# Kernel optimization log

Measured on AMD Instinct MI355X. Metric: run time of the kernel, lower is better.

The kernel has to match this reference:

```python
import jax, jax.numpy as jnp
import numpy as np

N_NODES = 100000
N_EDGES = 600000
EMB = 128
L = 5
NUM_ATOM = 119
NUM_CHIR = 3
NUM_BTYPE = 5
NUM_BDIR = 3
BN_EPS = 1e-5


def setup_inputs() -> dict:
    key = jax.random.key(0)
    ks = jax.random.split(key, 16)
    inp = {}
    inp['x'] = jax.random.randint(ks[0], (N_NODES, 2), 0, NUM_ATOM, dtype=jnp.int64 if jax.config.jax_enable_x64 else jnp.int32)
    inp['edge_index'] = jax.random.randint(ks[1], (2, N_EDGES), 0, N_NODES)
    inp['edge_attr'] = jax.random.randint(ks[2], (N_EDGES, 2), 0, NUM_BDIR)
    s = 0.05
    inp['x_emb1'] = jax.random.normal(ks[3], (NUM_ATOM, EMB), jnp.float32) * s
    inp['x_emb2'] = jax.random.normal(ks[4], (NUM_CHIR, EMB), jnp.float32) * s
    inp['edge_emb1'] = jax.random.normal(ks[5], (L, NUM_BTYPE, EMB), jnp.float32) * s
    inp['edge_emb2'] = jax.random.normal(ks[6], (L, NUM_BDIR, EMB), jnp.float32) * s
    inp['W1'] = jax.random.normal(ks[7], (L, EMB, 2 * EMB), jnp.float32) * (1.0 / np.sqrt(EMB))
    inp['b1'] = jnp.zeros((L, 2 * EMB), jnp.float32)
    inp['W2'] = jax.random.normal(ks[8], (L, 2 * EMB, EMB), jnp.float32) * (1.0 / np.sqrt(2 * EMB))
    inp['b2'] = jnp.zeros((L, EMB), jnp.float32)
    inp['eps'] = jnp.zeros((L,), jnp.float32)
    inp['gamma'] = jnp.ones((L, EMB), jnp.float32)
    inp['beta'] = jnp.zeros((L, EMB), jnp.float32)
    return inp


def reference(x, edge_index, edge_attr, x_emb1, x_emb2, edge_emb1, edge_emb2,
              W1, b1, W2, b2, eps, gamma, beta):
    N = x.shape[0]
    # node embedding: sum of two table lookups
    x0 = jnp.clip(x[:, 0], 0, x_emb1.shape[0] - 1)
    x1 = jnp.clip(x[:, 1], 0, x_emb2.shape[0] - 1)
    h = x_emb1[x0] + x_emb2[x1]  # [N, EMB]
    # add self loops (loop edge_attr = zeros -> bond type 0 / dir 0)
    loop = jnp.arange(N, dtype=edge_index.dtype)
    src = jnp.concatenate([edge_index[0], loop])  # [E+N]
    dst = jnp.concatenate([edge_index[1], loop])
    ea = jnp.concatenate([edge_attr, jnp.zeros((N, 2), dtype=edge_attr.dtype)], axis=0)
    e0 = jnp.clip(ea[:, 0], 0, edge_emb1.shape[1] - 1)
    e1 = jnp.clip(ea[:, 1], 0, edge_emb2.shape[1] - 1)
    n_layers = eps.shape[0]
    for i in range(n_layers):
        e = edge_emb1[i][e0] + edge_emb2[i][e1]              # [E+N, EMB]
        m = jax.nn.relu(h[src] + e)                           # gather + elementwise
        agg = jax.ops.segment_sum(m, dst, num_segments=N)     # scatter-add
        out = (1.0 + eps[i]) * h + agg
        # MLP: Linear -> ReLU -> Linear
        hmid = jax.nn.relu(out @ W1[i] + b1[i])
        h = hmid @ W2[i] + b2[i]
        # BatchNorm1d over nodes (batch statistics, biased variance)
        mean = jnp.mean(h, axis=0)
        var = jnp.mean((h - mean) ** 2, axis=0)
        h = (h - mean) * jax.lax.rsqrt(var + BN_EPS) * gamma[i] + beta[i]
        if i < n_layers - 1:
            h = jax.nn.relu(h)
    return h
```

## Files before the change

### kernel.cpp

```cpp
#include <hip/hip_runtime.h>

#define NN 100000
#define NPAD 100096
#define NE 600000
#define EMB 128

typedef unsigned short u16;
typedef unsigned int u32;
typedef unsigned long long u64;
typedef _Float16 half8 __attribute__((ext_vector_type(8)));
typedef float f32x4 __attribute__((ext_vector_type(4)));

__device__ __forceinline__ float4 ld4(const float* p) { return *(const float4*)p; }
__device__ __forceinline__ u32 packh2(float a, float b) {
  union { _Float16 h[2]; u32 d; } u;
  u.h[0] = (_Float16)a;
  u.h[1] = (_Float16)b;
  return u.d;
}

__global__ __launch_bounds__(256) void node_init_kernel(
    const int* __restrict__ x, const float* __restrict__ emb1,
    const float* __restrict__ emb2, _Float16* __restrict__ hb) {
  int tid = blockIdx.x * blockDim.x + threadIdx.x;
  int n = tid >> 4;
  if (n >= NN) return;
  int kc = tid & 15;
  int x0 = min(max(x[2 * n], 0), 118);
  int x1 = min(max(x[2 * n + 1], 0), 2);
  const float* p1 = emb1 + (size_t)x0 * EMB + kc * 8;
  const float* p2 = emb2 + (size_t)x1 * EMB + kc * 8;
  _Float16 o[8];
#pragma unroll
  for (int j = 0; j < 8; ++j) o[j] = (_Float16)(p1[j] + p2[j]);
  *(ulonglong2*)(hb + (size_t)n * EMB + kc * 8) = *(ulonglong2*)o;
}

__global__ __launch_bounds__(256) void hist_kernel(const int* __restrict__ ei,
                                                   int* __restrict__ deg) {
  int e = blockIdx.x * blockDim.x + threadIdx.x;
  if (e >= NE) return;
  atomicAdd(&deg[ei[NE + e]], 1);
}

__global__ __launch_bounds__(256) void scan1_kernel(const int* __restrict__ deg,
                                                    int* __restrict__ off,
                                                    int* __restrict__ bsum) {
  __shared__ int s[256];
  int t = threadIdx.x;
  int base = blockIdx.x * 1024 + t * 4;
  int v[4];
#pragma unroll
  for (int j = 0; j < 4; ++j) {
    int idx = base + j;
    v[j] = (idx < NN) ? deg[idx] : 0;
  }
  int tsum = v[0] + v[1] + v[2] + v[3];
  s[t] = tsum;
  __syncthreads();
  for (int d = 1; d < 256; d <<= 1) {
    int add = (t >= d) ? s[t - d] : 0;
    __syncthreads();
    s[t] += add;
    __syncthreads();
  }
  int run = s[t] - tsum;
#pragma unroll
  for (int j = 0; j < 4; ++j) {
    int idx = base + j;
    if (idx < NN) off[idx] = run;
    run += v[j];
  }
  if (t == 255) bsum[blockIdx.x] = s[255];
}

__global__ void scan2_kernel(int* __restrict__ bsum, int* __restrict__ off, int nb) {
  int lane = threadIdx.x;
  int v0 = (lane < nb) ? bsum[lane] : 0;
  int v1 = (lane + 64 < nb) ? bsum[lane + 64] : 0;
  int s0 = v0, s1 = v1;
  for (int d = 1; d < 64; d <<= 1) {
    int t0 = __shfl_up(s0, d);
    int t1 = __shfl_up(s1, d);
    if (lane >= d) { s0 += t0; s1 += t1; }
  }
  int tot0 = __shfl(s0, 63);
  int tot1 = __shfl(s1, 63);
  if (lane < nb) bsum[lane] = s0 - v0;
  if (lane + 64 < nb) bsum[lane + 64] = tot0 + s1 - v1;
  if (lane == 0) off[NN] = tot0 + tot1;
}

__global__ __launch_bounds__(256) void scan3_kernel(int* __restrict__ off,
                                                    const int* __restrict__ bsum) {
  int idx = blockIdx.x * blockDim.x + threadIdx.x;
  if (idx < NN) off[idx] += bsum[idx >> 10];
}

__global__ __launch_bounds__(256) void scatter_kernel(
    const int* __restrict__ ei, const int* __restrict__ ea,
    const int* __restrict__ off, int* __restrict__ cnt, int* __restrict__ csr) {
  int e = blockIdx.x * blockDim.x + threadIdx.x;
  if (e >= NE) return;
  int d = ei[NE + e];
  int s = ei[e];
  int a0 = min(max(ea[2 * e], 0), 4);
  int a1 = min(max(ea[2 * e + 1], 0), 2);
  int code = a0 * 3 + a1;
  int r = atomicAdd(&cnt[d], 1);
  csr[off[d] + r] = s | (code << 20);
}

__global__ __launch_bounds__(256) void dhist_kernel(const int* __restrict__ deg,
                                                    int* __restrict__ gbins) {
  __shared__ int l[33];
  int t = threadIdx.x;
  if (t < 33) l[t] = 0;
  __syncthreads();
  int n = blockIdx.x * 256 + t;
  if (n < NN) atomicAdd(&l[32 - min(deg[n], 32)], 1);
  __syncthreads();
  if (t < 33 && l[t]) atomicAdd(&gbins[t], l[t]);
}

__global__ void dscan_kernel(int* __restrict__ gbins) {
  int lane = threadIdx.x;
  int v = (lane < 33) ? gbins[lane] : 0;
  int s = v;
  for (int d = 1; d < 64; d <<= 1) {
    int t = __shfl_up(s, d);
    if (lane >= d) s += t;
  }
  if (lane < 33) gbins[lane] = s - v;
}

__global__ __launch_bounds__(256) void dscatter_kernel(const int* __restrict__ deg,
                                                       int* __restrict__ gbins,
                                                       int* __restrict__ perm) {
  __shared__ int lcnt[33], lbase[33];
  int t = threadIdx.x;
  if (t < 33) lcnt[t] = 0;
  __syncthreads();
  int n = blockIdx.x * 256 + t;
  int b = 0, r = 0;
  if (n < NN) {
    b = 32 - min(deg[n], 32);
    r = atomicAdd(&lcnt[b], 1);
  }
  __syncthreads();
  if (t < 33) lbase[t] = lcnt[t] ? atomicAdd(&gbins[t], lcnt[t]) : 0;
  __syncthreads();
  if (n < NN) perm[lbase[b] + r] = n;
}

__global__ __launch_bounds__(256) void combo_kernel(const float* __restrict__ ee1,
                                                    const float* __restrict__ ee2,
                                                    _Float16* __restrict__ cbh) {
  int idx = blockIdx.x * blockDim.x + threadIdx.x;
  if (idx >= 5 * 15 * 128) return;
  int l = idx / (15 * 128);
  int rem = idx % (15 * 128);
  int code = rem / 128;
  int f = rem % 128;
  cbh[idx] = (_Float16)(ee1[(l * 5 + code / 3) * 128 + f] + ee2[(l * 3 + code % 3) * 128 + f]);
}

__global__ __launch_bounds__(256) void prep_w_kernel(
    const float* __restrict__ W1g, const float* __restrict__ W2g,
    _Float16* __restrict__ W1f, _Float16* __restrict__ W2f) {
  int idx = blockIdx.x * blockDim.x + threadIdx.x;
  if (idx >= 40960) return;
  _Float16 o[8];
  if (idx < 20480) {
    int lane = idx & 63;
    int r = idx >> 6;
    int nt = r & 3, kt = (r >> 2) & 3, c = (r >> 4) & 3, l = r >> 6;
    int n = c * 64 + nt * 16 + (lane & 15);
    int kb = kt * 32 + (lane >> 4) * 8;
#pragma unroll
    for (int j = 0; j < 8; ++j) o[j] = (_Float16)W1g[((size_t)l * 128 + kb + j) * 256 + n];
    *(ulonglong2*)(W1f + (size_t)idx * 8) = *(ulonglong2*)o;
  } else {
    int i2 = idx - 20480;
    int lane = i2 & 63;
    int r = i2 >> 6;
    int nt = r & 7, ktl = (r >> 3) & 1, c = (r >> 4) & 3, l = r >> 6;
    int n = nt * 16 + (lane & 15);
    int kb = c * 64 + ktl * 32 + (lane >> 4) * 8;
#pragma unroll
    for (int j = 0; j < 8; ++j) o[j] = (_Float16)W2g[((size_t)l * 256 + kb + j) * 128 + n];
    *(ulonglong2*)(W2f + (size_t)i2 * 8) = *(ulonglong2*)o;
  }
}

template <bool NORM>
__global__ __launch_bounds__(256) void agg_kernel(
    const _Float16* __restrict__ hsrc, const float* __restrict__ scsh,
    const int* __restrict__ off, const int* __restrict__ csr,
    const _Float16* __restrict__ cbh, const float* __restrict__ epsp,
    const int* __restrict__ perm, _Float16* __restrict__ Af) {
  int tid = blockIdx.x * blockDim.x + threadIdx.x;
  int g = tid >> 4;
  int kc = tid & 15;
  float av[8] = {0.f, 0.f, 0.f, 0.f, 0.f, 0.f, 0.f, 0.f};
  float scv[8], shv[8];
  if (NORM) {
    float4 sa = ld4(scsh + kc * 8), sb = ld4(scsh + kc * 8 + 4);
    float4 ha = ld4(scsh + 128 + kc * 8), hbv = ld4(scsh + 128 + kc * 8 + 4);
    scv[0] = sa.x; scv[1] = sa.y; scv[2] = sa.z; scv[3] = sa.w;
    scv[4] = sb.x; scv[5] = sb.y; scv[6] = sb.z; scv[7] = sb.w;
    shv[0] = ha.x; shv[1] = ha.y; shv[2] = ha.z; shv[3] = ha.w;
    shv[4] = hbv.x; shv[5] = hbv.y; shv[6] = hbv.z; shv[7] = hbv.w;
  }
  int node = g;
  if (g < NN) {
    node = perm[g];
    const float eps1 = 1.0f + *epsp;
    ulonglong2 hraw = *(const ulonglong2*)(hsrc + (size_t)node * EMB + kc * 8);
    _Float16* hr = (_Float16*)&hraw;
    half8 c0 = *(const half8*)(cbh + kc * 8);
#pragma unroll
    for (int j = 0; j < 8; ++j) {
      float hv = (float)hr[j];
      if (NORM) hv = fmaxf(hv * scv[j] + shv[j], 0.f);
      av[j] = eps1 * hv + fmaxf(hv + (float)c0[j], 0.f);
    }
    int s0 = off[node], s1 = off[node + 1];
    int e = s0;
    for (; e + 3 < s1; e += 4) {
      int p0 = csr[e], p1 = csr[e + 1], p2 = csr[e + 2], p3 = csr[e + 3];
      ulonglong2 r0 = *(const ulonglong2*)(hsrc + (size_t)(p0 & 0xFFFFF) * EMB + kc * 8);
      ulonglong2 r1 = *(const ulonglong2*)(hsrc + (size_t)(p1 & 0xFFFFF) * EMB + kc * 8);
      ulonglong2 r2 = *(const ulonglong2*)(hsrc + (size_t)(p2 & 0xFFFFF) * EMB + kc * 8);
      ulonglong2 r3 = *(const ulonglong2*)(hsrc + (size_t)(p3 & 0xFFFFF) * EMB + kc * 8);
      ulonglong2 rr[4] = {r0, r1, r2, r3};
      int pp[4] = {p0, p1, p2, p3};
#pragma unroll
      for (int u = 0; u < 4; ++u) {
        half8 cc = *(const half8*)(cbh + (size_t)(pp[u] >> 20) * EMB + kc * 8);
        _Float16* sp = (_Float16*)&rr[u];
#pragma unroll
        for (int j = 0; j < 8; ++j) {
          float v = (float)sp[j];
          if (NORM) v = fmaxf(v * scv[j] + shv[j], 0.f);
          av[j] += fmaxf(v + (float)cc[j], 0.f);
        }
      }
    }
    for (; e < s1; ++e) {
      int p0 = csr[e];
      ulonglong2 r0 = *(const ulonglong2*)(hsrc + (size_t)(p0 & 0xFFFFF) * EMB + kc * 8);
      half8 cc = *(const half8*)(cbh + (size_t)(p0 >> 20) * EMB + kc * 8);
      _Float16* sp = (_Float16*)&r0;
#pragma unroll
      for (int j = 0; j < 8; ++j) {
        float v = (float)sp[j];
        if (NORM) v = fmaxf(v * scv[j] + shv[j], 0.f);
        av[j] += fmaxf(v + (float)cc[j], 0.f);
      }
    }
  }
  _Float16 o[8];
#pragma unroll
  for (int j = 0; j < 8; ++j) o[j] = (_Float16)av[j];
  *(ulonglong2*)(Af + (size_t)node * EMB + kc * 8) = *(ulonglong2*)o;
}

__global__ __launch_bounds__(256, 4) void mlp_kernel(
    const _Float16* __restrict__ Af, const _Float16* __restrict__ W1f,
    const _Float16* __restrict__ W2f,
    const float* __restrict__ b1g, const float* __restrict__ b2g,
    _Float16* __restrict__ hpre, float* __restrict__ slots) {
  __shared__ __align__(16) _Float16 Ws[16 * 64 * 8];

  const int t = threadIdx.x;
  const int w = t >> 6;
  const int lane = t & 63;
  const int q = lane >> 4, l15 = lane & 15;
  const int gw = blockIdx.x * 4 + w;
  const int n0 = gw * 16;
  float* sums = slots + (size_t)(gw & 31) * 256;

  half8 nh[4];
#pragma unroll
  for (int kt = 0; kt < 4; ++kt)
    nh[kt] = *(const half8*)(Af + (size_t)(n0 + l15) * EMB + kt * 32 + q * 8);

  f32x4 oacc[8];
#pragma unroll
  for (int a = 0; a < 8; ++a) oacc[a] = (f32x4){0.f, 0.f, 0.f, 0.f};

  const int srcA = ((q & 1) * 2) * 16 + l15;
  const int srcB = srcA + 16;
  const bool sel = (q >> 1) != 0;

  for (int c = 0; c < 4; ++c) {
    __syncthreads();
    {
      const _Float16* gb = W1f + ((size_t)(c * 16 + w * 4) * 64 + lane) * 8;
#pragma unroll
      for (int j = 0; j < 4; ++j)
        *(ulonglong2*)&Ws[(w * 4 + j) * 512 + lane * 8] =
            *(const ulonglong2*)(gb + (size_t)j * 512);
    }
    __syncthreads();

    f32x4 hacc[4];
#pragma unroll
    for (int a = 0; a < 4; ++a) hacc[a] = (f32x4){0.f, 0.f, 0.f, 0.f};
#pragma unroll
    for (int kt = 0; kt < 4; ++kt) {
#pragma unroll
      for (int colt = 0; colt < 4; ++colt) {
        half8 wh = *(const half8*)&Ws[(kt * 4 + colt) * 512 + lane * 8];
        hacc[colt] = __builtin_amdgcn_mfma_f32_16x16x32_f16(wh, nh[kt], hacc[colt], 0, 0, 0);
      }
    }
    __syncthreads();

    {
      const _Float16* gb = W2f + ((size_t)(c * 16 + w * 4) * 64 + lane) * 8;
#pragma unroll
      for (int j = 0; j < 4; ++j)
        *(ulonglong2*)&Ws[(w * 4 + j) * 512 + lane * 8] =
            *(const ulonglong2*)(gb + (size_t)j * 512);
    }

    u32 P01[4], P23[4];
#pragma unroll
    for (int colt = 0; colt < 4; ++colt) {
      float4 b1v = ld4(b1g + c * 64 + colt * 16 + q * 4);
      float v0 = fmaxf(hacc[colt][0] + b1v.x, 0.f);
      float v1 = fmaxf(hacc[colt][1] + b1v.y, 0.f);
      float v2 = fmaxf(hacc[colt][2] + b1v.z, 0.f);
      float v3 = fmaxf(hacc[colt][3] + b1v.w, 0.f);
      P01[colt] = packh2(v0, v1);
      P23[colt] = packh2(v2, v3);
    }
    __syncthreads();

#pragma unroll
    for (int ktl = 0; ktl < 2; ++ktl) {
      half8 bh;
      {
        union { u32 d[4]; half8 s; } uh;
        int c0 = 2 * ktl, c1 = 2 * ktl + 1;
        u32 a0, a1;
        a0 = (u32)__shfl((int)P01[c0], srcA); a1 = (u32)__shfl((int)P01[c1], srcA);
        uh.d[0] = sel ? a1 : a0;
        a0 = (u32)__shfl((int)P23[c0], srcA); a1 = (u32)__shfl((int)P23[c1], srcA);
        uh.d[1] = sel ? a1 : a0;
        a0 = (u32)__shfl((int)P01[c0], srcB); a1 = (u32)__shfl((int)P01[c1], srcB);
        uh.d[2] = sel ? a1 : a0;
        a0 = (u32)__shfl((int)P23[c0], srcB); a1 = (u32)__shfl((int)P23[c1], srcB);
        uh.d[3] = sel ? a1 : a0;
        bh = uh.s;
      }
#pragma unroll
      for (int nt = 0; nt < 8; ++nt) {
        half8 wh = *(const half8*)&Ws[(ktl * 8 + nt) * 512 + lane * 8];
        oacc[nt] = __builtin_amdgcn_mfma_f32_16x16x32_f16(wh, bh, oacc[nt], 0, 0, 0);
      }
    }
  }

  const int node = n0 + l15;
#pragma unroll
  for (int nt = 0; nt < 8; ++nt) {
    int ocb = nt * 16 + q * 4;
    float4 b2v = ld4(b2g + ocb);
    f32x4 s = (f32x4){0.f, 0.f, 0.f, 0.f};
    f32x4 s2 = (f32x4){0.f, 0.f, 0.f, 0.f};
    if (node < NN) {
      float v0 = oacc[nt][0] + b2v.x;
      float v1 = oacc[nt][1] + b2v.y;
      float v2 = oacc[nt][2] + b2v.z;
      float v3 = oacc[nt][3] + b2v.w;
      u64 pk = (u64)packh2(v0, v1) | ((u64)packh2(v2, v3) << 32);
      *(u64*)(hpre + (size_t)node * EMB + ocb) = pk;
      s[0] = v0; s[1] = v1; s[2] = v2; s[3] = v3;
      s2[0] = v0 * v0; s2[1] = v1 * v1; s2[2] = v2 * v2; s2[3] = v3 * v3;
    }
#pragma unroll
    for (int d = 1; d < 16; d <<= 1) {
#pragma unroll
      for (int r = 0; r < 4; ++r) {
        s[r] += __shfl_xor(s[r], d);
        s2[r] += __shfl_xor(s2[r], d);
      }
    }
    if (l15 == 0) {
#pragma unroll
      for (int r = 0; r < 4; ++r) {
        atomicAdd(&sums[ocb + r], s[r]);
        atomicAdd(&sums[128 + ocb + r], s2[r]);
      }
    }
  }
}

__global__ void stats_kernel(const float* __restrict__ slots,
                             const float* __restrict__ gamma,
                             const float* __restrict__ beta,
                             float* __restrict__ scsh) {
  int f = threadIdx.x;
  float s = 0.f, s2 = 0.f;
#pragma unroll 8
  for (int k = 0; k < 32; ++k) {
    s += slots[k * 256 + f];
    s2 += slots[k * 256 + 128 + f];
  }
  float mean = s * (1.0f / NN);
  float var = s2 * (1.0f / NN) - mean * mean;
  float sc = gamma[f] * rsqrtf(var + 1e-5f);
  scsh[f] = sc;
  scsh[128 + f] = beta[f] - mean * sc;
}

__global__ __launch_bounds__(256) void out_kernel(
    const _Float16* __restrict__ hpre, const float* __restrict__ scsh,
    float* __restrict__ out) {
  int tid = blockIdx.x * blockDim.x + threadIdx.x;
  int n = tid >> 4;
  if (n >= NN) return;
  int kc = tid & 15;
  ulonglong2 raw = *(const ulonglong2*)(hpre + (size_t)n * EMB + kc * 8);
  _Float16* hr = (_Float16*)&raw;
  float4 sa = ld4(scsh + kc * 8), sb = ld4(scsh + kc * 8 + 4);
  float4 ha = ld4(scsh + 128 + kc * 8), hbv = ld4(scsh + 128 + kc * 8 + 4);
  float scv[8] = {sa.x, sa.y, sa.z, sa.w, sb.x, sb.y, sb.z, sb.w};
  float shv[8] = {ha.x, ha.y, ha.z, ha.w, hbv.x, hbv.y, hbv.z, hbv.w};
  float v[8];
#pragma unroll
  for (int j = 0; j < 8; ++j) v[j] = (float)hr[j] * scv[j] + shv[j];
  float* d = out + (size_t)n * EMB + kc * 8;
  *(float4*)d = make_float4(v[0], v[1], v[2], v[3]);
  *(float4*)(d + 4) = make_float4(v[4], v[5], v[6], v[7]);
}

extern "C" void kernel_launch(void* const* d_in, const int* in_sizes, int n_in,
                              void* d_out, int out_size, void* d_ws, size_t ws_size,
                              hipStream_t stream) {
  const int* x = (const int*)d_in[0];
  const int* ei = (const int*)d_in[1];
  const int* ea = (const int*)d_in[2];
  const float* x_emb1 = (const float*)d_in[3];
  const float* x_emb2 = (const float*)d_in[4];
  const float* ee1 = (const float*)d_in[5];
  const float* ee2 = (const float*)d_in[6];
  const float* W1 = (const float*)d_in[7];
  const float* b1 = (const float*)d_in[8];
  const float* W2 = (const float*)d_in[9];
  const float* b2 = (const float*)d_in[10];
  const float* eps = (const float*)d_in[11];
  const float* gamma = (const float*)d_in[12];
  const float* beta = (const float*)d_in[13];
  float* out = (float*)d_out;

  float* slots = (float*)d_ws;
  float* scsh = slots + 5 * 32 * 256;
  _Float16* hpre = (_Float16*)(scsh + 5 * 256);
  _Float16* Af = hpre + (size_t)NN * EMB;
  _Float16* hb = Af + (size_t)NPAD * EMB;
  _Float16* W1f = hb + (size_t)NN * EMB;
  _Float16* W2f = W1f + 5 * 32768;
  _Float16* cbh = W2f + 5 * 32768;
  int* deg = (int*)(cbh + 5 * 15 * 128 + 64);
  int* off = deg + NN;
  int* csr = off + NN + 1;
  int* bsum = csr + NE;
  int* gbins = bsum + 128;
  int* perm = gbins + 64;

  const int NB_SCAN = (NN + 1023) / 1024;

  hipMemsetAsync(deg, 0, NN * sizeof(int), stream);
  hipMemsetAsync(gbins, 0, 64 * sizeof(int), stream);
  hipMemsetAsync(slots, 0, 5 * 32 * 256 * sizeof(float), stream);
  hist_kernel<<<(NE + 255) / 256, 256, 0, stream>>>(ei, deg);
  dhist_kernel<<<(NN + 255) / 256, 256, 0, stream>>>(deg, gbins);
  dscan_kernel<<<1, 64, 0, stream>>>(gbins);
  dscatter_kernel<<<(NN + 255) / 256, 256, 0, stream>>>(deg, gbins, perm);
  scan1_kernel<<<NB_SCAN, 256, 0, stream>>>(deg, off, bsum);
  scan2_kernel<<<1, 64, 0, stream>>>(bsum, off, NB_SCAN);
  scan3_kernel<<<(NN + 255) / 256, 256, 0, stream>>>(off, bsum);
  hipMemsetAsync(deg, 0, NN * sizeof(int), stream);
  scatter_kernel<<<(NE + 255) / 256, 256, 0, stream>>>(ei, ea, off, deg, csr);
  combo_kernel<<<(5 * 15 * 128 + 255) / 256, 256, 0, stream>>>(ee1, ee2, cbh);
  prep_w_kernel<<<160, 256, 0, stream>>>(W1, W2, W1f, W2f);
  node_init_kernel<<<NN * 16 / 256 + 1, 256, 0, stream>>>(x, x_emb1, x_emb2, hb);

  const int NBLK = NPAD / 64;
  for (int i = 0; i < 5; ++i) {
    if (i == 0)
      agg_kernel<false><<<NPAD * 16 / 256, 256, 0, stream>>>(
          hb, nullptr, off, csr, cbh + (size_t)i * 15 * EMB, eps + i, perm, Af);
    else
      agg_kernel<true><<<NPAD * 16 / 256, 256, 0, stream>>>(
          hpre, scsh + (size_t)(i - 1) * 256, off, csr,
          cbh + (size_t)i * 15 * EMB, eps + i, perm, Af);
    mlp_kernel<<<NBLK, 256, 0, stream>>>(
        Af, W1f + (size_t)i * 32768, W2f + (size_t)i * 32768,
        b1 + (size_t)i * 256, b2 + (size_t)i * 128, hpre,
        slots + (size_t)i * 32 * 256);
    stats_kernel<<<1, 128, 0, stream>>>(slots + (size_t)i * 32 * 256,
                                        gamma + (size_t)i * EMB,
                                        beta + (size_t)i * EMB,
                                        scsh + (size_t)i * 256);
  }
  out_kernel<<<NN * 16 / 256 + 1, 256, 0, stream>>>(hpre, scsh + 4 * 256, out);
}
```

Before: 644.1 us.

## Fuse preprocessing kernels, fold BN stats into consumers, drop MLP LDS weight staging

The degree-histogram, scan and permutation kernels are merged into the existing scan1/scan2/scan3 kernels, and the combo and weight prep kernels become one prep kernel. The per-layer stats kernel is removed: every block of agg_kernel and out_kernel now recomputes the BatchNorm scale and shift from the slot partial sums into shared memory. The MLP kernel no longer stages weights through LDS with barriers and reads fragments straight from global memory or L2. The aim is fewer launches and no barriers, at the cost of redundant per-block stats reduction and more global weight traffic in the MLP.

```diff
diff --git a/kernel.cpp b/kernel.cpp
--- a/kernel.cpp
+++ b/kernel.cpp
@@ -45,9 +45,12 @@
 
 __global__ __launch_bounds__(256) void scan1_kernel(const int* __restrict__ deg,
                                                     int* __restrict__ off,
-                                                    int* __restrict__ bsum) {
+                                                    int* __restrict__ bsum,
+                                                    int* __restrict__ gbins) {
   __shared__ int s[256];
+  __shared__ int l[33];
   int t = threadIdx.x;
+  if (t < 33) l[t] = 0;
   int base = blockIdx.x * 1024 + t * 4;
   int v[4];
 #pragma unroll
@@ -68,33 +71,67 @@
 #pragma unroll
   for (int j = 0; j < 4; ++j) {
     int idx = base + j;
-    if (idx < NN) off[idx] = run;
+    if (idx < NN) {
+      off[idx] = run;
+      atomicAdd(&l[32 - min(v[j], 32)], 1);
+    }
     run += v[j];
   }
   if (t == 255) bsum[blockIdx.x] = s[255];
-}
-
-__global__ void scan2_kernel(int* __restrict__ bsum, int* __restrict__ off, int nb) {
-  int lane = threadIdx.x;
-  int v0 = (lane < nb) ? bsum[lane] : 0;
-  int v1 = (lane + 64 < nb) ? bsum[lane + 64] : 0;
-  int s0 = v0, s1 = v1;
-  for (int d = 1; d < 64; d <<= 1) {
-    int t0 = __shfl_up(s0, d);
-    int t1 = __shfl_up(s1, d);
-    if (lane >= d) { s0 += t0; s1 += t1; }
-  }
-  int tot0 = __shfl(s0, 63);
-  int tot1 = __shfl(s1, 63);
-  if (lane < nb) bsum[lane] = s0 - v0;
-  if (lane + 64 < nb) bsum[lane + 64] = tot0 + s1 - v1;
-  if (lane == 0) off[NN] = tot0 + tot1;
+  __syncthreads();
+  if (t < 33 && l[t]) atomicAdd(&gbins[t], l[t]);
+}
+
+__global__ void scan2_kernel(int* __restrict__ bsum, int* __restrict__ off, int nb,
+                             int* __restrict__ gbins) {
+  int t = threadIdx.x;
+  if (t < 64) {
+    int lane = t;
+    int v0 = (lane < nb) ? bsum[lane] : 0;
+    int v1 = (lane + 64 < nb) ? bsum[lane + 64] : 0;
+    int s0 = v0, s1 = v1;
+    for (int d = 1; d < 64; d <<= 1) {
+      int t0 = __shfl_up(s0, d);
+      int t1 = __shfl_up(s1, d);
+      if (lane >= d) { s0 += t0; s1 += t1; }
+    }
+    int tot0 = __shfl(s0, 63);
+    int tot1 = __shfl(s1, 63);
+    if (lane < nb) bsum[lane] = s0 - v0;
+    if (lane + 64 < nb) bsum[lane + 64] = tot0 + s1 - v1;
+    if (lane == 0) off[NN] = tot0 + tot1;
+  } else {
+    int lane = t - 64;
+    int v = (lane < 33) ? gbins[lane] : 0;
+    int s = v;
+    for (int d = 1; d < 64; d <<= 1) {
+      int tt = __shfl_up(s, d);
+      if (lane >= d) s += tt;
+    }
+    if (lane < 33) gbins[lane] = s - v;
+  }
 }
 
 __global__ __launch_bounds__(256) void scan3_kernel(int* __restrict__ off,
-                                                    const int* __restrict__ bsum) {
-  int idx = blockIdx.x * blockDim.x + threadIdx.x;
-  if (idx < NN) off[idx] += bsum[idx >> 10];
+                                                    const int* __restrict__ bsum,
+                                                    const int* __restrict__ deg,
+                                                    int* __restrict__ gbins,
+                                                    int* __restrict__ perm) {
+  __shared__ int lcnt[33], lbase[33];
+  int t = threadIdx.x;
+  if (t < 33) lcnt[t] = 0;
+  __syncthreads();
+  int idx = blockIdx.x * 256 + t;
+  int b = 0, r = 0;
+  if (idx < NN) {
+    off[idx] += bsum[idx >> 10];
+    b = 32 - min(deg[idx], 32);
+    r = atomicAdd(&lcnt[b], 1);
+  }
+  __syncthreads();
+  if (t < 33) lbase[t] = lcnt[t] ? atomicAdd(&gbins[t], lcnt[t]) : 0;
+  __syncthreads();
+  if (idx < NN) perm[lbase[b] + r] = idx;
 }
 
 __global__ __launch_bounds__(256) void scatter_kernel(
@@ -111,65 +148,12 @@
   csr[off[d] + r] = s | (code << 20);
 }
 
-__global__ __launch_bounds__(256) void dhist_kernel(const int* __restrict__ deg,
-                                                    int* __restrict__ gbins) {
-  __shared__ int l[33];
-  int t = threadIdx.x;
-  if (t < 33) l[t] = 0;
-  __syncthreads();
-  int n = blockIdx.x * 256 + t;
-  if (n < NN) atomicAdd(&l[32 - min(deg[n], 32)], 1);
-  __syncthreads();
-  if (t < 33 && l[t]) atomicAdd(&gbins[t], l[t]);
-}
-
-__global__ void dscan_kernel(int* __restrict__ gbins) {
-  int lane = threadIdx.x;
-  int v = (lane < 33) ? gbins[lane] : 0;
-  int s = v;
-  for (int d = 1; d < 64; d <<= 1) {
-    int t = __shfl_up(s, d);
-    if (lane >= d) s += t;
-  }
-  if (lane < 33) gbins[lane] = s - v;
-}
-
-__global__ __launch_bounds__(256) void dscatter_kernel(const int* __restrict__ deg,
-                                                       int* __restrict__ gbins,
-                                                       int* __restrict__ perm) {
-  __shared__ int lcnt[33], lbase[33];
-  int t = threadIdx.x;
-  if (t < 33) lcnt[t] = 0;
-  __syncthreads();
-  int n = blockIdx.x * 256 + t;
-  int b = 0, r = 0;
-  if (n < NN) {
-    b = 32 - min(deg[n], 32);
-    r = atomicAdd(&lcnt[b], 1);
-  }
-  __syncthreads();
-  if (t < 33) lbase[t] = lcnt[t] ? atomicAdd(&gbins[t], lcnt[t]) : 0;
-  __syncthreads();
-  if (n < NN) perm[lbase[b] + r] = n;
-}
-
-__global__ __launch_bounds__(256) void combo_kernel(const float* __restrict__ ee1,
-                                                    const float* __restrict__ ee2,
-                                                    _Float16* __restrict__ cbh) {
+__global__ __launch_bounds__(256) void prep_kernel(
+    const float* __restrict__ W1g, const float* __restrict__ W2g,
+    const float* __restrict__ ee1, const float* __restrict__ ee2,
+    _Float16* __restrict__ W1f, _Float16* __restrict__ W2f,
+    _Float16* __restrict__ cbh) {
   int idx = blockIdx.x * blockDim.x + threadIdx.x;
-  if (idx >= 5 * 15 * 128) return;
-  int l = idx / (15 * 128);
-  int rem = idx % (15 * 128);
-  int code = rem / 128;
-  int f = rem % 128;
-  cbh[idx] = (_Float16)(ee1[(l * 5 + code / 3) * 128 + f] + ee2[(l * 3 + code % 3) * 128 + f]);
-}
-
-__global__ __launch_bounds__(256) void prep_w_kernel(
-    const float* __restrict__ W1g, const float* __restrict__ W2g,
-    _Float16* __restrict__ W1f, _Float16* __restrict__ W2f) {
-  int idx = blockIdx.x * blockDim.x + threadIdx.x;
-  if (idx >= 40960) return;
   _Float16 o[8];
   if (idx < 20480) {
     int lane = idx & 63;
@@ -180,7 +164,7 @@
 #pragma unroll
     for (int j = 0; j < 8; ++j) o[j] = (_Float16)W1g[((size_t)l * 128 + kb + j) * 256 + n];
     *(ulonglong2*)(W1f + (size_t)idx * 8) = *(ulonglong2*)o;
-  } else {
+  } else if (idx < 40960) {
     int i2 = idx - 20480;
     int lane = i2 & 63;
     int r = i2 >> 6;
@@ -190,27 +174,52 @@
 #pragma unroll
     for (int j = 0; j < 8; ++j) o[j] = (_Float16)W2g[((size_t)l * 256 + kb + j) * 128 + n];
     *(ulonglong2*)(W2f + (size_t)i2 * 8) = *(ulonglong2*)o;
+  } else if (idx < 40960 + 9600) {
+    int i3 = idx - 40960;
+    int l = i3 / (15 * 128);
+    int rem = i3 % (15 * 128);
+    int code = rem / 128;
+    int f = rem % 128;
+    cbh[i3] = (_Float16)(ee1[(l * 5 + code / 3) * 128 + f] + ee2[(l * 3 + code % 3) * 128 + f]);
   }
 }
 
 template <bool NORM>
 __global__ __launch_bounds__(256) void agg_kernel(
-    const _Float16* __restrict__ hsrc, const float* __restrict__ scsh,
+    const _Float16* __restrict__ hsrc, const float* __restrict__ slots,
+    const float* __restrict__ gamma, const float* __restrict__ beta,
     const int* __restrict__ off, const int* __restrict__ csr,
     const _Float16* __restrict__ cbh, const float* __restrict__ epsp,
     const int* __restrict__ perm, _Float16* __restrict__ Af) {
-  int tid = blockIdx.x * blockDim.x + threadIdx.x;
+  __shared__ float s_sc[128], s_sh[128];
+  int t = threadIdx.x;
+  if (NORM) {
+    if (t < 128) {
+      float s = 0.f, s2 = 0.f;
+#pragma unroll 8
+      for (int k = 0; k < 32; ++k) {
+        s += slots[k * 256 + t];
+        s2 += slots[k * 256 + 128 + t];
+      }
+      float mean = s * (1.0f / NN);
+      float var = s2 * (1.0f / NN) - mean * mean;
+      float sc = gamma[t] * rsqrtf(var + 1e-5f);
+      s_sc[t] = sc;
+      s_sh[t] = beta[t] - mean * sc;
+    }
+    __syncthreads();
+  }
+  int tid = blockIdx.x * blockDim.x + t;
   int g = tid >> 4;
   int kc = tid & 15;
   float av[8] = {0.f, 0.f, 0.f, 0.f, 0.f, 0.f, 0.f, 0.f};
   float scv[8], shv[8];
   if (NORM) {
-    float4 sa = ld4(scsh + kc * 8), sb = ld4(scsh + kc * 8 + 4);
-    float4 ha = ld4(scsh + 128 + kc * 8), hbv = ld4(scsh + 128 + kc * 8 + 4);
-    scv[0] = sa.x; scv[1] = sa.y; scv[2] = sa.z; scv[3] = sa.w;
-    scv[4] = sb.x; scv[5] = sb.y; scv[6] = sb.z; scv[7] = sb.w;
-    shv[0] = ha.x; shv[1] = ha.y; shv[2] = ha.z; shv[3] = ha.w;
-    shv[4] = hbv.x; shv[5] = hbv.y; shv[6] = hbv.z; shv[7] = hbv.w;
+#pragma unroll
+    for (int j = 0; j < 8; ++j) {
+      scv[j] = s_sc[kc * 8 + j];
+      shv[j] = s_sh[kc * 8 + j];
+    }
   }
   int node = g;
   if (g < NN) {
@@ -271,8 +280,6 @@
     const _Float16* __restrict__ W2f,
     const float* __restrict__ b1g, const float* __restrict__ b2g,
     _Float16* __restrict__ hpre, float* __restrict__ slots) {
-  __shared__ __align__(16) _Float16 Ws[16 * 64 * 8];
-
   const int t = threadIdx.x;
   const int w = t >> 6;
   const int lane = t & 63;
@@ -281,6 +288,9 @@
   const int n0 = gw * 16;
   float* sums = slots + (size_t)(gw & 31) * 256;
 
+  const half8* W1v = (const half8*)W1f;
+  const half8* W2v = (const half8*)W2f;
+
   half8 nh[4];
 #pragma unroll
   for (int kt = 0; kt < 4; ++kt)
@@ -294,17 +304,8 @@
   const int srcB = srcA + 16;
   const bool sel = (q >> 1) != 0;
 
+#pragma unroll
   for (int c = 0; c < 4; ++c) {
-    __syncthreads();
-    {
-      const _Float16* gb = W1f + ((size_t)(c * 16 + w * 4) * 64 + lane) * 8;
-#pragma unroll
-      for (int j = 0; j < 4; ++j)
-        *(ulonglong2*)&Ws[(w * 4 + j) * 512 + lane * 8] =
-            *(const ulonglong2*)(gb + (size_t)j * 512);
-    }
-    __syncthreads();
-
     f32x4 hacc[4];
 #pragma unroll
     for (int a = 0; a < 4; ++a) hacc[a] = (f32x4){0.f, 0.f, 0.f, 0.f};
@@ -312,18 +313,9 @@
     for (int kt = 0; kt < 4; ++kt) {
 #pragma unroll
       for (int colt = 0; colt < 4; ++colt) {
-        half8 wh = *(const half8*)&Ws[(kt * 4 + colt) * 512 + lane * 8];
+        half8 wh = W1v[(size_t)(c * 16 + kt * 4 + colt) * 64 + lane];
         hacc[colt] = __builtin_amdgcn_mfma_f32_16x16x32_f16(wh, nh[kt], hacc[colt], 0, 0, 0);
       }
-    }
-    __syncthreads();
-
-    {
-      const _Float16* gb = W2f + ((size_t)(c * 16 + w * 4) * 64 + lane) * 8;
-#pragma unroll
-      for (int j = 0; j < 4; ++j)
-        *(ulonglong2*)&Ws[(w * 4 + j) * 512 + lane * 8] =
-            *(const ulonglong2*)(gb + (size_t)j * 512);
     }
 
     u32 P01[4], P23[4];
@@ -337,7 +329,6 @@
       P01[colt] = packh2(v0, v1);
       P23[colt] = packh2(v2, v3);
     }
-    __syncthreads();
 
 #pragma unroll
     for (int ktl = 0; ktl < 2; ++ktl) {
@@ -358,7 +349,7 @@
       }
 #pragma unroll
       for (int nt = 0; nt < 8; ++nt) {
-        half8 wh = *(const half8*)&Ws[(ktl * 8 + nt) * 512 + lane * 8];
+        half8 wh = W2v[(size_t)(c * 16 + ktl * 8 + nt) * 64 + lane];
         oacc[nt] = __builtin_amdgcn_mfma_f32_16x16x32_f16(wh, bh, oacc[nt], 0, 0, 0);
       }
     }
@@ -399,40 +390,35 @@
   }
 }
 
-__global__ void stats_kernel(const float* __restrict__ slots,
-                             const float* __restrict__ gamma,
-                             const float* __restrict__ beta,
-                             float* __restrict__ scsh) {
-  int f = threadIdx.x;
-  float s = 0.f, s2 = 0.f;
+__global__ __launch_bounds__(256) void out_kernel(
+    const _Float16* __restrict__ hpre, const float* __restrict__ slots,
+    const float* __restrict__ gamma, const float* __restrict__ beta,
+    float* __restrict__ out) {
+  __shared__ float s_sc[128], s_sh[128];
+  int t = threadIdx.x;
+  if (t < 128) {
+    float s = 0.f, s2 = 0.f;
 #pragma unroll 8
-  for (int k = 0; k < 32; ++k) {
-    s += slots[k * 256 + f];
-    s2 += slots[k * 256 + 128 + f];
-  }
-  float mean = s * (1.0f / NN);
-  float var = s2 * (1.0f / NN) - mean * mean;
-  float sc = gamma[f] * rsqrtf(var + 1e-5f);
-  scsh[f] = sc;
-  scsh[128 + f] = beta[f] - mean * sc;
-}
-
-__global__ __launch_bounds__(256) void out_kernel(
-    const _Float16* __restrict__ hpre, const float* __restrict__ scsh,
-    float* __restrict__ out) {
-  int tid = blockIdx.x * blockDim.x + threadIdx.x;
+    for (int k = 0; k < 32; ++k) {
+      s += slots[k * 256 + t];
+      s2 += slots[k * 256 + 128 + t];
+    }
+    float mean = s * (1.0f / NN);
+    float var = s2 * (1.0f / NN) - mean * mean;
+    float sc = gamma[t] * rsqrtf(var + 1e-5f);
+    s_sc[t] = sc;
+    s_sh[t] = beta[t] - mean * sc;
+  }
+  __syncthreads();
+  int tid = blockIdx.x * blockDim.x + t;
   int n = tid >> 4;
   if (n >= NN) return;
   int kc = tid & 15;
   ulonglong2 raw = *(const ulonglong2*)(hpre + (size_t)n * EMB + kc * 8);
   _Float16* hr = (_Float16*)&raw;
-  float4 sa = ld4(scsh + kc * 8), sb = ld4(scsh + kc * 8 + 4);
-  float4 ha = ld4(scsh + 128 + kc * 8), hbv = ld4(scsh + 128 + kc * 8 + 4);
-  float scv[8] = {sa.x, sa.y, sa.z, sa.w, sb.x, sb.y, sb.z, sb.w};
-  float shv[8] = {ha.x, ha.y, ha.z, ha.w, hbv.x, hbv.y, hbv.z, hbv.w};
   float v[8];
 #pragma unroll
-  for (int j = 0; j < 8; ++j) v[j] = (float)hr[j] * scv[j] + shv[j];
+  for (int j = 0; j < 8; ++j) v[j] = (float)hr[j] * s_sc[kc * 8 + j] + s_sh[kc * 8 + j];
   float* d = out + (size_t)n * EMB + kc * 8;
   *(float4*)d = make_float4(v[0], v[1], v[2], v[3]);
   *(float4*)(d + 4) = make_float4(v[4], v[5], v[6], v[7]);
@@ -458,8 +444,7 @@
   float* out = (float*)d_out;
 
   float* slots = (float*)d_ws;
-  float* scsh = slots + 5 * 32 * 256;
-  _Float16* hpre = (_Float16*)(scsh + 5 * 256);
+  _Float16* hpre = (_Float16*)(slots + 5 * 32 * 256);
   _Float16* Af = hpre + (size_t)NN * EMB;
   _Float16* hb = Af + (size_t)NPAD * EMB;
   _Float16* W1f = hb + (size_t)NN * EMB;
@@ -478,35 +463,31 @@
   hipMemsetAsync(gbins, 0, 64 * sizeof(int), stream);
   hipMemsetAsync(slots, 0, 5 * 32 * 256 * sizeof(float), stream);
   hist_kernel<<<(NE + 255) / 256, 256, 0, stream>>>(ei, deg);
-  dhist_kernel<<<(NN + 255) / 256, 256, 0, stream>>>(deg, gbins);
-  dscan_kernel<<<1, 64, 0, stream>>>(gbins);
-  dscatter_kernel<<<(NN + 255) / 256, 256, 0, stream>>>(deg, gbins, perm);
-  scan1_kernel<<<NB_SCAN, 256, 0, stream>>>(deg, off, bsum);
-  scan2_kernel<<<1, 64, 0, stream>>>(bsum, off, NB_SCAN);
-  scan3_kernel<<<(NN + 255) / 256, 256, 0, stream>>>(off, bsum);
+  scan1_kernel<<<NB_SCAN, 256, 0, stream>>>(deg, off, bsum, gbins);
+  scan2_kernel<<<1, 128, 0, stream>>>(bsum, off, NB_SCAN, gbins);
+  scan3_kernel<<<(NN + 255) / 256, 256, 0, stream>>>(off, bsum, deg, gbins, perm);
   hipMemsetAsync(deg, 0, NN * sizeof(int), stream);
   scatter_kernel<<<(NE + 255) / 256, 256, 0, stream>>>(ei, ea, off, deg, csr);
-  combo_kernel<<<(5 * 15 * 128 + 255) / 256, 256, 0, stream>>>(ee1, ee2, cbh);
-  prep_w_kernel<<<160, 256, 0, stream>>>(W1, W2, W1f, W2f);
+  prep_kernel<<<(40960 + 9600 + 255) / 256, 256, 0, stream>>>(W1, W2, ee1, ee2, W1f,
+                                                              W2f, cbh);
   node_init_kernel<<<NN * 16 / 256 + 1, 256, 0, stream>>>(x, x_emb1, x_emb2, hb);
 
   const int NBLK = NPAD / 64;
   for (int i = 0; i < 5; ++i) {
     if (i == 0)
       agg_kernel<false><<<NPAD * 16 / 256, 256, 0, stream>>>(
-          hb, nullptr, off, csr, cbh + (size_t)i * 15 * EMB, eps + i, perm, Af);
+          hb, nullptr, nullptr, nullptr, off, csr, cbh + (size_t)i * 15 * EMB,
+          eps + i, perm, Af);
     else
       agg_kernel<true><<<NPAD * 16 / 256, 256, 0, stream>>>(
-          hpre, scsh + (size_t)(i - 1) * 256, off, csr,
-          cbh + (size_t)i * 15 * EMB, eps + i, perm, Af);
+          hpre, slots + (size_t)(i - 1) * 32 * 256, gamma + (size_t)(i - 1) * EMB,
+          beta + (size_t)(i - 1) * EMB, off, csr, cbh + (size_t)i * 15 * EMB,
+          eps + i, perm, Af);
     mlp_kernel<<<NBLK, 256, 0, stream>>>(
         Af, W1f + (size_t)i * 32768, W2f + (size_t)i * 32768,
         b1 + (size_t)i * 256, b2 + (size_t)i * 128, hpre,
         slots + (size_t)i * 32 * 256);
-    stats_kernel<<<1, 128, 0, stream>>>(slots + (size_t)i * 32 * 256,
-                                        gamma + (size_t)i * EMB,
-                                        beta + (size_t)i * EMB,
-                                        scsh + (size_t)i * 256);
-  }
-  out_kernel<<<NN * 16 / 256 + 1, 256, 0, stream>>>(hpre, scsh + 4 * 256, out);
-}
+  }
+  out_kernel<<<NN * 16 / 256 + 1, 256, 0, stream>>>(
+      hpre, slots + 4 * 32 * 256, gamma + 4 * EMB, beta + 4 * EMB, out);
+}
```

Measured after the change: 793.4 us. 1.23x slower.
